# Optimization experiments

Hardware: AMD Instinct MI355X
Metric: run time of the kernel (lower is better)

The kernel has to match this reference:

```python
import jax, jax.numpy as jnp
import numpy as np

B, S, DM = 2, 2048, 2048
H, KV, HD = 16, 4, 128
THETA = 10000.0
EPS = 1e-6


def _rmsnorm(x, scale):
    # flax nnx.RMSNorm with dtype=float32: x / sqrt(mean(x^2)+eps) * scale
    var = jnp.mean(jnp.square(x.astype(jnp.float32)), axis=-1, keepdims=True)
    return (x.astype(jnp.float32) * jax.lax.rsqrt(var + EPS)) * scale


def _apply_rope(x, positions, base):
    # x: [B, S, heads, HD]; positions: [1, S]
    half = HD // 2
    fraction = 2.0 * jnp.arange(half, dtype=jnp.float32) / HD
    timescale = base ** fraction                              # [HD/2]
    sinusoid = positions[..., None].astype(jnp.float32) / timescale  # [1, S, HD/2]
    sinusoid = sinusoid[..., None, :]                         # [1, S, 1, HD/2]
    sin, cos = jnp.sin(sinusoid), jnp.cos(sinusoid)
    x1, x2 = x[..., :half], x[..., half:]
    return jnp.concatenate([x1 * cos - x2 * sin, x2 * cos + x1 * sin], axis=-1).astype(x.dtype)


def setup_inputs() -> dict:
    key = jax.random.key(0)
    ks = jax.random.split(key, 7)
    w = lambda k, shape: jax.random.normal(k, shape, jnp.float32) * 0.02
    return {
        "x": jax.random.normal(ks[0], (B, S, DM), jnp.float32),
        "wq": w(ks[1], (DM, H, HD)),
        "wk": w(ks[2], (DM, KV, HD)),
        "wv": w(ks[3], (DM, KV, HD)),
        "wo": w(ks[4], (H, HD, DM)),
        "q_scale": jnp.ones((HD,), jnp.float32),
        "k_scale": jnp.ones((HD,), jnp.float32),
    }


def reference(x, wq, wk, wv, wo, q_scale, k_scale):
    # QKV projections (LinearGeneral hidden -> (heads, head_dim))
    q = jnp.einsum("bsd,dhk->bshk", x, wq)   # [B,S,H,HD]
    k = jnp.einsum("bsd,dhk->bshk", x, wk)   # [B,S,KV,HD]
    v = jnp.einsum("bsd,dhk->bshk", x, wv)   # [B,S,KV,HD]
    # qk RMSNorm + cast back to compute dtype
    q = _rmsnorm(q, q_scale).astype(x.dtype)
    k = _rmsnorm(k, k_scale).astype(x.dtype)
    # RoPE
    positions = jnp.arange(S)[None, :]
    q = _apply_rope(q, positions, THETA)
    k = _apply_rope(k, positions, THETA)
    # GQA attention: group query heads per kv head instead of materializing repeat_kv
    G = H // KV
    qg = q.reshape(B, S, KV, G, HD) * (HD ** -0.5)
    scores = jnp.einsum("bqkgd,bskd->bkgqs", qg, k)           # [B,KV,G,S,S]
    causal = jnp.tril(jnp.ones((S, S), jnp.bool_))
    scores = jnp.where(causal, scores, jnp.finfo(scores.dtype).min)
    probs = jax.nn.softmax(scores, axis=-1)
    att = jnp.einsum("bkgqs,bskd->bqkgd", probs, v).reshape(B, S, H, HD)
    # output projection contracting (heads, head_dim)
    return jnp.einsum("bshd,hdo->bso", att, wo)
```

## Files before the change

### kernel.cpp

```cpp
#include <hip/hip_runtime.h>
#include <hip/hip_bf16.h>
#include <math.h>

typedef unsigned short u16;
typedef short short8 __attribute__((ext_vector_type(8)));
typedef float floatx4 __attribute__((ext_vector_type(4)));

#define B_   2
#define S_   2048
#define DM_  2048
#define H_   16
#define KVH_ 4
#define HD_  128

__device__ __forceinline__ float bf2f(u16 v) {
  union { unsigned int u; float f; } x; x.u = ((unsigned int)v) << 16; return x.f;
}
__device__ __forceinline__ u16 f2bf(float f) {
  union { float f; unsigned int u; } x; x.f = f;
  unsigned int u = x.u;
  u += 0x7FFFu + ((u >> 16) & 1u);
  return (u16)(u >> 16);
}

#define GLDS16(gp, lp) __builtin_amdgcn_global_load_lds( \
    (const __attribute__((address_space(1))) unsigned int*)(const void*)(gp), \
    (__attribute__((address_space(3))) unsigned int*)(void*)(lp), 16, 0, 0)

__global__ __launch_bounds__(256) void k_prep(
    const float* __restrict__ x, const float* __restrict__ wq,
    const float* __restrict__ wk, const float* __restrict__ wv,
    const float* __restrict__ wo,
    u16* __restrict__ x_bf, u16* __restrict__ wqkv_t, u16* __restrict__ wo_t,
    float2* __restrict__ rope_tab)
{
  int bx = blockIdx.x;
  if (bx >= 18432) {
    int idx = (bx - 18432) * 256 + threadIdx.x;
    int pos = idx >> 6;
    float fi = (float)(idx & 63);
    float ts = powf(10000.0f, fi * (1.0f / 64.0f));
    float ang = (float)pos / ts;
    rope_tab[idx] = make_float2(cosf(ang), sinf(ang));
    return;
  }
  if (bx < 8192) {
    int i = bx * 256 + threadIdx.x;
    const float4 v = ((const float4*)x)[i];
    u16 o[4] = { f2bf(v.x), f2bf(v.y), f2bf(v.z), f2bf(v.w) };
    *(unsigned long long*)(x_bf + (size_t)i * 4) = *(unsigned long long*)o;
    return;
  }
  bx -= 8192;
  const float* src; u16* dst; int C, cb;
  if (bx < 4096)      { src = wq; dst = wqkv_t; C = 2048; cb = 64; }
  else if (bx < 5120) { bx -= 4096; src = wk; dst = wqkv_t + (size_t)2048 * 2048; C = 512; cb = 16; }
  else if (bx < 6144) { bx -= 5120; src = wv; dst = wqkv_t + (size_t)2560 * 2048; C = 512; cb = 16; }
  else                { bx -= 6144; src = wo; dst = wo_t; C = 2048; cb = 64; }
  const int R = 2048;
  int c0 = (bx % cb) * 32, r0 = (bx / cb) * 32;
  __shared__ float tile[32][33];
  int tx = threadIdx.x & 31, ty = threadIdx.x >> 5;
#pragma unroll
  for (int j = 0; j < 4; j++)
    tile[ty * 4 + j][tx] = src[(size_t)(r0 + ty * 4 + j) * C + c0 + tx];
  __syncthreads();
#pragma unroll
  for (int j = 0; j < 4; j++)
    dst[(size_t)(c0 + ty * 4 + j) * R + r0 + tx] = f2bf(tile[tx][ty * 4 + j]);
}

__global__ __launch_bounds__(256, 3) void k_gemm_bt(
    const u16* __restrict__ A, const u16* __restrict__ Bt,
    void* __restrict__ Cout, int M, int N, int K, int c_bf16)
{
  __shared__ u16 As[128 * 64];
  __shared__ u16 Bs[128 * 64];
  int tid = threadIdx.x;
  int lane = tid & 63;
  int quad = lane >> 4, l16 = lane & 15;
  int wid = tid >> 6;
  int m0 = blockIdx.y * 128, n0 = blockIdx.x * 128;
  int wm = (wid >> 1) * 64, wn = (wid & 1) * 64;

  floatx4 acc[4][4] = {};

  int srow = tid >> 3;
  int gjc0 = (tid & 7) ^ (srow & 7);
  const u16* Ap = A + (size_t)(m0 + srow) * K + gjc0 * 8;
  const u16* Bp = Bt + (size_t)(n0 + srow) * K + gjc0 * 8;
  u16* AsW = As + tid * 8;
  u16* BsW = Bs + tid * 8;

  for (int kt = 0; kt < K; kt += 64) {
    __syncthreads();
#pragma unroll
    for (int j = 0; j < 4; j++) {
      GLDS16(Ap + (size_t)(j * 32) * K, AsW + j * 2048);
      GLDS16(Bp + (size_t)(j * 32) * K, BsW + j * 2048);
    }
    Ap += 64; Bp += 64;
    __syncthreads();

#pragma unroll
    for (int ks = 0; ks < 2; ks++) {
      short8 af[4], bfv[4];
#pragma unroll
      for (int mi = 0; mi < 4; mi++) {
        int row = wm + mi * 16 + l16;
        af[mi] = *(const short8*)&As[row * 64 + (((ks * 4 + quad) ^ (row & 7)) * 8)];
      }
#pragma unroll
      for (int ni = 0; ni < 4; ni++) {
        int row = wn + ni * 16 + l16;
        bfv[ni] = *(const short8*)&Bs[row * 64 + (((ks * 4 + quad) ^ (row & 7)) * 8)];
      }
#pragma unroll
      for (int mi = 0; mi < 4; mi++)
#pragma unroll
        for (int ni = 0; ni < 4; ni++)
          acc[mi][ni] = __builtin_amdgcn_mfma_f32_16x16x32_bf16(
              af[mi], bfv[ni], acc[mi][ni], 0, 0, 0);
    }
  }

#pragma unroll
  for (int mi = 0; mi < 4; mi++)
#pragma unroll
    for (int ni = 0; ni < 4; ni++)
#pragma unroll
      for (int r = 0; r < 4; r++) {
        int row = m0 + wm + mi * 16 + quad * 4 + r;
        int col = n0 + wn + ni * 16 + l16;
        float v = acc[mi][ni][r];
        if (c_bf16) ((u16*)Cout)[(size_t)row * N + col] = f2bf(v);
        else        ((float*)Cout)[(size_t)row * N + col] = v;
      }
}

__global__ __launch_bounds__(256, 3) void k_gemm_qkv(
    const u16* __restrict__ A, const u16* __restrict__ Bt,
    const float* __restrict__ qs, const float* __restrict__ ks,
    const float2* __restrict__ tab,
    u16* __restrict__ qr, u16* __restrict__ kr, u16* __restrict__ vt)
{
  const int K = 2048;
  __shared__ u16 smem[16384] __attribute__((aligned(16)));
  u16* As = smem;
  u16* Bs = smem + 8192;
  float* exch = (float*)smem;

  int tid = threadIdx.x;
  int lane = tid & 63;
  int quad = lane >> 4, l16 = lane & 15;
  int wid = tid >> 6;
  int m0 = blockIdx.y * 128, n0 = blockIdx.x * 128;
  int wm = (wid >> 1) * 64, wn = (wid & 1) * 64;

  floatx4 acc[4][4] = {};

  int srow = tid >> 3;
  int gjc0 = (tid & 7) ^ (srow & 7);
  const u16* Ap = A + (size_t)(m0 + srow) * K + gjc0 * 8;
  const u16* Bp = Bt + (size_t)(n0 + srow) * K + gjc0 * 8;
  u16* AsW = As + tid * 8;
  u16* BsW = Bs + tid * 8;

  for (int kt = 0; kt < K; kt += 64) {
    __syncthreads();
#pragma unroll
    for (int j = 0; j < 4; j++) {
      GLDS16(Ap + (size_t)(j * 32) * K, AsW + j * 2048);
      GLDS16(Bp + (size_t)(j * 32) * K, BsW + j * 2048);
    }
    Ap += 64; Bp += 64;
    __syncthreads();

#pragma unroll
    for (int ks = 0; ks < 2; ks++) {
      short8 af[4], bfv[4];
#pragma unroll
      for (int mi = 0; mi < 4; mi++) {
        int row = wm + mi * 16 + l16;
        af[mi] = *(const short8*)&As[row * 64 + (((ks * 4 + quad) ^ (row & 7)) * 8)];
      }
#pragma unroll
      for (int ni = 0; ni < 4; ni++) {
        int row = wn + ni * 16 + l16;
        bfv[ni] = *(const short8*)&Bs[row * 64 + (((ks * 4 + quad) ^ (row & 7)) * 8)];
      }
#pragma unroll
      for (int mi = 0; mi < 4; mi++)
#pragma unroll
        for (int ni = 0; ni < 4; ni++)
          acc[mi][ni] = __builtin_amdgcn_mfma_f32_16x16x32_bf16(
              af[mi], bfv[ni], acc[mi][ni], 0, 0, 0);
    }
  }

  int nt = blockIdx.x;
  if (nt >= 20) {
    int kv = nt - 20;
    int b  = m0 >> 11;
    int s0 = m0 & (S_ - 1);
    __syncthreads();
#pragma unroll
    for (int mi = 0; mi < 4; mi++)
#pragma unroll
      for (int ni = 0; ni < 4; ni++)
#pragma unroll
        for (int r = 0; r < 4; r++) {
          int sl  = wm + mi * 16 + quad * 4 + r;
          int col = wn + ni * 16 + l16;
          smem[col * 128 + (((sl >> 3) ^ (col & 7)) * 8) + (sl & 7)] =
              f2bf(acc[mi][ni][r]);
        }
    __syncthreads();
    size_t vbase = ((size_t)(b * KVH_ + kv) * HD_) * S_ + s0;
#pragma unroll
    for (int i = 0; i < 8; i++) {
      int flat = i * 256 + tid;
      int hd = flat >> 4, sc = flat & 15;
      short8 vv = *(const short8*)&smem[hd * 128 + ((sc ^ (hd & 7)) * 8)];
      *(short8*)(vt + vbase + (size_t)hd * S_ + sc * 8) = vv;
    }
    return;
  }

  bool isq = nt < 16;
  const float* scp = isq ? qs : ks;
  float sc_own[4], sc_par[4];
#pragma unroll
  for (int ni = 0; ni < 4; ni++) {
    sc_own[ni] = scp[wn + ni * 16 + l16];
    sc_par[ni] = scp[(wn ^ 64) + ni * 16 + l16];
  }
  float ssign = (wn == 0) ? -1.0f : 1.0f;

#pragma unroll
  for (int mi = 0; mi < 4; mi++) {
    __syncthreads();
#pragma unroll
    for (int ni = 0; ni < 4; ni++)
#pragma unroll
      for (int r = 0; r < 4; r++)
        exch[(ni * 4 + r) * 256 + wid * 64 + lane] = acc[mi][ni][r];
    __syncthreads();
    float part[4][4];
#pragma unroll
    for (int ni = 0; ni < 4; ni++)
#pragma unroll
      for (int r = 0; r < 4; r++)
        part[ni][r] = exch[(ni * 4 + r) * 256 + (wid ^ 1) * 64 + lane];

#pragma unroll
    for (int r = 0; r < 4; r++) {
      float ss = 0.f;
#pragma unroll
      for (int ni = 0; ni < 4; ni++)
        ss += acc[mi][ni][r] * acc[mi][ni][r] + part[ni][r] * part[ni][r];
#pragma unroll
      for (int d = 1; d < 16; d <<= 1) ss += __shfl_xor(ss, d);
      float rs = rsqrtf(ss * (1.0f / 128.0f) + 1e-6f);
      int row = m0 + wm + mi * 16 + quad * 4 + r;
      int pos = row & (S_ - 1);
#pragma unroll
      for (int ni = 0; ni < 4; ni++) {
        float2 cs = tab[pos * 64 + ni * 16 + l16];
        float yo = acc[mi][ni][r] * rs * sc_own[ni];
        float yp = part[ni][r] * rs * sc_par[ni];
        float o = fmaf(ssign * yp, cs.y, yo * cs.x);
        if (isq) o *= 0.088388347648318447f;
        int d = wn + ni * 16 + l16;
        if (isq) qr[((size_t)row * H_ + nt) * HD_ + d] = f2bf(o);
        else     kr[((size_t)row * KVH_ + (nt - 16)) * HD_ + d] = f2bf(o);
      }
    }
  }
}

__global__ __launch_bounds__(256, 2) void k_flash(
    const u16* __restrict__ qr, const u16* __restrict__ kr,
    const u16* __restrict__ vt, u16* __restrict__ att)
{
  __shared__ u16 smem[40960] __attribute__((aligned(16)));
  u16* Ps = smem + 32768;
  float* lpbuf = (float*)(smem + 32768);

  int tid = threadIdx.x, lane = tid & 63, wid = tid >> 6;
  int quad = lane >> 4, l16 = lane & 15;
  int rhalf = wid & 1;
  int shalf = wid >> 1;
  int bx = blockIdx.x;
  int it = 31 - (bx >> 5);
  int hb = bx & 31;
  int h = hb & 15, b = hb >> 4;
  int kvh = h >> 2;
  int q0 = it * 64;
  int NT = it + 1;

  short8 qf[2][4];
#pragma unroll
  for (int m = 0; m < 2; m++) {
    const u16* qb = qr + ((size_t)(b * S_ + q0 + rhalf * 32 + m * 16 + l16) * H_ + h) * HD_;
#pragma unroll
    for (int kk = 0; kk < 4; kk++)
      qf[m][kk] = *(const short8*)(qb + kk * 32 + quad * 8);
  }

  int gjk = (tid & 15) ^ ((tid >> 4) & 15);
  int gjv = (tid & 7) ^ ((tid >> 3) & 7);
  const u16* kp = kr + ((size_t)(b * S_ + (tid >> 4)) * KVH_ + kvh) * HD_ + gjk * 8;
  const u16* vp = vt + ((size_t)(b * KVH_ + kvh) * HD_ + (tid >> 3)) * S_ + gjv * 8;

#pragma unroll
  for (int j = 0; j < 4; j++) {
    GLDS16(kp + (size_t)(j * 16) * KVH_ * HD_, smem + (size_t)(j * 256 + tid) * 8);
    GLDS16(vp + (size_t)(j * 32) * S_,         smem + 16384 + (size_t)(j * 256 + tid) * 8);
  }
  kp += (size_t)64 * KVH_ * HD_;
  vp += 64;
  __syncthreads();

  floatx4 accO[2][8] = {};
  float lp[2][4] = {};
  u16* PsW = Ps + wid * 2048;

  const float LOG2E = 1.4426950408889634f;
  const float MBIAS = -12.5f * 1.4426950408889634f;
  int qmax = q0 + rhalf * 32 + 31;

  for (int kt = 0; kt < NT; kt++) {
    if (kt + 1 < NT) {
      u16* KD = smem + (size_t)((kt + 1) & 1) * 8192;
      u16* VD = smem + 16384 + (size_t)((kt + 1) & 1) * 8192;
#pragma unroll
      for (int j = 0; j < 4; j++) {
        GLDS16(kp + (size_t)(j * 16) * KVH_ * HD_, KD + (size_t)(j * 256 + tid) * 8);
        GLDS16(vp + (size_t)(j * 32) * S_,         VD + (size_t)(j * 256 + tid) * 8);
      }
      kp += (size_t)64 * KVH_ * HD_;
      vp += 64;
    }

    int k0 = kt * 64;
    int s0w = k0 + shalf * 32;
    if (s0w <= qmax) {
      const u16* KsC = smem + (size_t)(kt & 1) * 8192;
      const u16* VtC = smem + 16384 + (size_t)(kt & 1) * 8192;

      floatx4 sacc[2][2] = {};
      __builtin_amdgcn_s_setprio(1);
#pragma unroll
      for (int kk = 0; kk < 4; kk++) {
        short8 kf[2];
#pragma unroll
        for (int nt = 0; nt < 2; nt++) {
          int row = shalf * 32 + nt * 16 + l16;
          kf[nt] = *(const short8*)&KsC[row * 128 + (((kk * 4 + quad) ^ (row & 15)) * 8)];
        }
#pragma unroll
        for (int nt = 0; nt < 2; nt++) {
          sacc[0][nt] = __builtin_amdgcn_mfma_f32_16x16x32_bf16(qf[0][kk], kf[nt], sacc[0][nt], 0, 0, 0);
          sacc[1][nt] = __builtin_amdgcn_mfma_f32_16x16x32_bf16(qf[1][kk], kf[nt], sacc[1][nt], 0, 0, 0);
        }
      }
      __builtin_amdgcn_s_setprio(0);

      bool diag = (s0w + 31 > q0 + rhalf * 32);
#pragma unroll
      for (int m = 0; m < 2; m++)
#pragma unroll
        for (int r = 0; r < 4; r++) {
          int prow = m * 16 + quad * 4 + r;
          int qrow = q0 + rhalf * 32 + prow;
          float rsum = 0.f;
#pragma unroll
          for (int nt = 0; nt < 2; nt++) {
            float p = __builtin_amdgcn_exp2f(fmaf(sacc[m][nt][r], LOG2E, MBIAS));
            if (diag && (s0w + nt * 16 + l16) > qrow) p = 0.f;
            rsum += p;
            int chunk = nt * 2 + (l16 >> 3);
            PsW[prow * 64 + ((chunk ^ (prow & 7)) * 8) + (l16 & 7)] = f2bf(p);
          }
          lp[m][r] += rsum;
        }

      __builtin_amdgcn_s_setprio(1);
      short8 pf[2];
#pragma unroll
      for (int m = 0; m < 2; m++) {
        int prow = m * 16 + l16;
        pf[m] = *(const short8*)&PsW[prow * 64 + ((quad ^ (prow & 7)) * 8)];
      }
#pragma unroll
      for (int ht = 0; ht < 8; ht++) {
        int row = ht * 16 + l16;
        short8 vf = *(const short8*)&VtC[row * 64 + (((shalf * 4 + quad) ^ (row & 7)) * 8)];
        accO[0][ht] = __builtin_amdgcn_mfma_f32_16x16x32_bf16(pf[0], vf, accO[0][ht], 0, 0, 0);
        accO[1][ht] = __builtin_amdgcn_mfma_f32_16x16x32_bf16(pf[1], vf, accO[1][ht], 0, 0, 0);
      }
      __builtin_amdgcn_s_setprio(0);
    }
    __syncthreads();
  }

#pragma unroll
  for (int m = 0; m < 2; m++)
#pragma unroll
    for (int r = 0; r < 4; r++) {
#pragma unroll
      for (int d = 1; d < 16; d <<= 1) lp[m][r] += __shfl_xor(lp[m][r], d);
    }

  floatx4* xch = (floatx4*)(void*)smem;
  if (wid >= 2) {
    floatx4* dst = xch + ((wid & 1) * 1024 + lane * 16);
#pragma unroll
    for (int m = 0; m < 2; m++)
#pragma unroll
      for (int ht = 0; ht < 8; ht++)
        dst[(m * 8 + ht + lane) & 15] = accO[m][ht];
    if (l16 == 0) {
#pragma unroll
      for (int m = 0; m < 2; m++)
#pragma unroll
        for (int r = 0; r < 4; r++)
          lpbuf[(wid & 1) * 32 + m * 16 + quad * 4 + r] = lp[m][r];
    }
  }
  __syncthreads();
  if (wid < 2) {
    floatx4* src = xch + (wid * 1024 + lane * 16);
    float inv[2][4];
#pragma unroll
    for (int m = 0; m < 2; m++)
#pragma unroll
      for (int ht = 0; ht < 8; ht++)
        accO[m][ht] += src[(m * 8 + ht + lane) & 15];
#pragma unroll
    for (int m = 0; m < 2; m++)
#pragma unroll
      for (int r = 0; r < 4; r++)
        inv[m][r] = 1.0f / (lp[m][r] + lpbuf[wid * 32 + m * 16 + quad * 4 + r]);
#pragma unroll
    for (int m = 0; m < 2; m++)
#pragma unroll
      for (int ht = 0; ht < 8; ht++)
#pragma unroll
        for (int r = 0; r < 4; r++) {
          int row = q0 + wid * 32 + m * 16 + quad * 4 + r;
          att[((size_t)(b * S_ + row) * H_ + h) * HD_ + ht * 16 + l16] =
              f2bf(accO[m][ht][r] * inv[m][r]);
        }
  }
}

extern "C" void kernel_launch(void* const* d_in, const int* in_sizes, int n_in,
                              void* d_out, int out_size, void* d_ws, size_t ws_size,
                              hipStream_t stream)
{
  const float* x  = (const float*)d_in[0];
  const float* wq = (const float*)d_in[1];
  const float* wk = (const float*)d_in[2];
  const float* wv = (const float*)d_in[3];
  const float* wo = (const float*)d_in[4];
  const float* qs = (const float*)d_in[5];
  const float* ks = (const float*)d_in[6];

  char* ws = (char*)d_ws;
  size_t off = 0;
  u16* x_bf   = (u16*)(ws + off); off += (size_t)4096 * 2048 * 2;
  u16* wqkv_t = (u16*)(ws + off); off += (size_t)3072 * 2048 * 2;
  u16* wo_t   = (u16*)(ws + off); off += (size_t)2048 * 2048 * 2;
  u16* q_rope = (u16*)(ws + off); off += (size_t)4096 * 16 * 128 * 2;
  u16* k_rope = (u16*)(ws + off); off += (size_t)4096 * 4 * 128 * 2;
  u16* vt     = (u16*)(ws + off); off += (size_t)8 * 128 * 2048 * 2;
  u16* att    = (u16*)(ws + off); off += (size_t)4096 * 2048 * 2;
  float2* rope_tab = (float2*)(ws + off); off += (size_t)2048 * 64 * 8;

  k_prep<<<dim3(18944), 256, 0, stream>>>(x, wq, wk, wv, wo, x_bf, wqkv_t, wo_t, rope_tab);

  k_gemm_qkv<<<dim3(24, 32), 256, 0, stream>>>(x_bf, wqkv_t, qs, ks, rope_tab,
                                               q_rope, k_rope, vt);

  k_flash<<<dim3(1024), 256, 0, stream>>>(q_rope, k_rope, vt, att);

  k_gemm_bt<<<dim3(16, 32), 256, 0, stream>>>(att, wo_t, d_out, 4096, 2048, 2048, 0);

  (void)in_sizes; (void)n_in; (void)out_size; (void)ws_size;
}
```

Before: 274.0 us.

## Keep softmax probabilities in registers by computing transposed S tile

Swaps MFMA operand order so each lane holds scores for one query row across consecutive keys, and permutes the K tile row loading so the register layout matches the PV MFMA A-operand. Probabilities are packed to bf16 with v_cvt_pk_bf16_f32 and fed directly to the PV MFMA, removing the per-wave LDS round trip for P and shrinking shared memory. Row sums become per-lane and need fewer shuffles, with a shuffle to redistribute them at the end. The risk is a subtle layout mismatch in the K-row permutation.

```diff
diff --git a/kernel.cpp b/kernel.cpp
--- a/kernel.cpp
+++ b/kernel.cpp
@@ -283,9 +283,8 @@
     const u16* __restrict__ qr, const u16* __restrict__ kr,
     const u16* __restrict__ vt, u16* __restrict__ att)
 {
-  __shared__ u16 smem[40960] __attribute__((aligned(16)));
-  u16* Ps = smem + 32768;
-  float* lpbuf = (float*)(smem + 32768);
+  __shared__ u16 smem[32768] __attribute__((aligned(16)));
+  float* lpbuf = (float*)(smem + 16384);
 
   int tid = threadIdx.x, lane = tid & 63, wid = tid >> 6;
   int quad = lane >> 4, l16 = lane & 15;
@@ -308,14 +307,17 @@
       qf[m][kk] = *(const short8*)(qb + kk * 32 + quad * 8);
   }
 
-  int gjk = (tid & 15) ^ ((tid >> 4) & 15);
+  int R0 = tid >> 4;
+  int base_act = (R0 >> 2) * 8 + (R0 & 3);
+  int gjk = (tid & 15) ^ (R0 & 15);
   int gjv = (tid & 7) ^ ((tid >> 3) & 7);
-  const u16* kp = kr + ((size_t)(b * S_ + (tid >> 4)) * KVH_ + kvh) * HD_ + gjk * 8;
+  const u16* kp = kr + ((size_t)(b * S_ + base_act) * KVH_ + kvh) * HD_ + gjk * 8;
   const u16* vp = vt + ((size_t)(b * KVH_ + kvh) * HD_ + (tid >> 3)) * S_ + gjv * 8;
+  const int joffK[4] = {0, 4, 32, 36};
 
 #pragma unroll
   for (int j = 0; j < 4; j++) {
-    GLDS16(kp + (size_t)(j * 16) * KVH_ * HD_, smem + (size_t)(j * 256 + tid) * 8);
+    GLDS16(kp + (size_t)joffK[j] * KVH_ * HD_, smem + (size_t)(j * 256 + tid) * 8);
     GLDS16(vp + (size_t)(j * 32) * S_,         smem + 16384 + (size_t)(j * 256 + tid) * 8);
   }
   kp += (size_t)64 * KVH_ * HD_;
@@ -323,12 +325,12 @@
   __syncthreads();
 
   floatx4 accO[2][8] = {};
-  float lp[2][4] = {};
-  u16* PsW = Ps + wid * 2048;
+  float lp[2] = { 0.f, 0.f };
 
   const float LOG2E = 1.4426950408889634f;
   const float MBIAS = -12.5f * 1.4426950408889634f;
   int qmax = q0 + rhalf * 32 + 31;
+  int qrow0 = q0 + rhalf * 32 + l16;
 
   for (int kt = 0; kt < NT; kt++) {
     if (kt + 1 < NT) {
@@ -336,7 +338,7 @@
       u16* VD = smem + 16384 + (size_t)((kt + 1) & 1) * 8192;
 #pragma unroll
       for (int j = 0; j < 4; j++) {
-        GLDS16(kp + (size_t)(j * 16) * KVH_ * HD_, KD + (size_t)(j * 256 + tid) * 8);
+        GLDS16(kp + (size_t)joffK[j] * KVH_ * HD_, KD + (size_t)(j * 256 + tid) * 8);
         GLDS16(vp + (size_t)(j * 32) * S_,         VD + (size_t)(j * 256 + tid) * 8);
       }
       kp += (size_t)64 * KVH_ * HD_;
@@ -361,38 +363,39 @@
         }
 #pragma unroll
         for (int nt = 0; nt < 2; nt++) {
-          sacc[0][nt] = __builtin_amdgcn_mfma_f32_16x16x32_bf16(qf[0][kk], kf[nt], sacc[0][nt], 0, 0, 0);
-          sacc[1][nt] = __builtin_amdgcn_mfma_f32_16x16x32_bf16(qf[1][kk], kf[nt], sacc[1][nt], 0, 0, 0);
+          sacc[0][nt] = __builtin_amdgcn_mfma_f32_16x16x32_bf16(kf[nt], qf[0][kk], sacc[0][nt], 0, 0, 0);
+          sacc[1][nt] = __builtin_amdgcn_mfma_f32_16x16x32_bf16(kf[nt], qf[1][kk], sacc[1][nt], 0, 0, 0);
         }
       }
       __builtin_amdgcn_s_setprio(0);
 
       bool diag = (s0w + 31 > q0 + rhalf * 32);
-#pragma unroll
-      for (int m = 0; m < 2; m++)
-#pragma unroll
-        for (int r = 0; r < 4; r++) {
-          int prow = m * 16 + quad * 4 + r;
-          int qrow = q0 + rhalf * 32 + prow;
-          float rsum = 0.f;
-#pragma unroll
-          for (int nt = 0; nt < 2; nt++) {
-            float p = __builtin_amdgcn_exp2f(fmaf(sacc[m][nt][r], LOG2E, MBIAS));
-            if (diag && (s0w + nt * 16 + l16) > qrow) p = 0.f;
+      int kb = s0w + quad * 8;
+      short8 pf[2];
+#pragma unroll
+      for (int m = 0; m < 2; m++) {
+        int qrow = qrow0 + m * 16;
+        float ps[8];
+        float rsum = 0.f;
+#pragma unroll
+        for (int nti = 0; nti < 2; nti++)
+#pragma unroll
+          for (int r = 0; r < 4; r++) {
+            float p = __builtin_amdgcn_exp2f(fmaf(sacc[m][nti][r], LOG2E, MBIAS));
+            if (diag && (kb + nti * 4 + r) > qrow) p = 0.f;
+            ps[nti * 4 + r] = p;
             rsum += p;
-            int chunk = nt * 2 + (l16 >> 3);
-            PsW[prow * 64 + ((chunk ^ (prow & 7)) * 8) + (l16 & 7)] = f2bf(p);
           }
-          lp[m][r] += rsum;
-        }
+        lp[m] += rsum;
+        union { unsigned int w[4]; short8 s; } pk_;
+#pragma unroll
+        for (int c = 0; c < 4; c++)
+          asm("v_cvt_pk_bf16_f32 %0, %1, %2"
+              : "=v"(pk_.w[c]) : "v"(ps[2 * c]), "v"(ps[2 * c + 1]));
+        pf[m] = pk_.s;
+      }
 
       __builtin_amdgcn_s_setprio(1);
-      short8 pf[2];
-#pragma unroll
-      for (int m = 0; m < 2; m++) {
-        int prow = m * 16 + l16;
-        pf[m] = *(const short8*)&PsW[prow * 64 + ((quad ^ (prow & 7)) * 8)];
-      }
 #pragma unroll
       for (int ht = 0; ht < 8; ht++) {
         int row = ht * 16 + l16;
@@ -406,12 +409,10 @@
   }
 
 #pragma unroll
-  for (int m = 0; m < 2; m++)
-#pragma unroll
-    for (int r = 0; r < 4; r++) {
-#pragma unroll
-      for (int d = 1; d < 16; d <<= 1) lp[m][r] += __shfl_xor(lp[m][r], d);
-    }
+  for (int m = 0; m < 2; m++) {
+    lp[m] += __shfl_xor(lp[m], 16);
+    lp[m] += __shfl_xor(lp[m], 32);
+  }
 
   floatx4* xch = (floatx4*)(void*)smem;
   if (wid >= 2) {
@@ -421,12 +422,10 @@
 #pragma unroll
       for (int ht = 0; ht < 8; ht++)
         dst[(m * 8 + ht + lane) & 15] = accO[m][ht];
-    if (l16 == 0) {
+    if (lane < 16) {
 #pragma unroll
       for (int m = 0; m < 2; m++)
-#pragma unroll
-        for (int r = 0; r < 4; r++)
-          lpbuf[(wid & 1) * 32 + m * 16 + quad * 4 + r] = lp[m][r];
+        lpbuf[(wid & 1) * 32 + m * 16 + lane] = lp[m];
     }
   }
   __syncthreads();
@@ -441,8 +440,10 @@
 #pragma unroll
     for (int m = 0; m < 2; m++)
 #pragma unroll
-      for (int r = 0; r < 4; r++)
-        inv[m][r] = 1.0f / (lp[m][r] + lpbuf[wid * 32 + m * 16 + quad * 4 + r]);
+      for (int r = 0; r < 4; r++) {
+        float own = __shfl(lp[m], quad * 4 + r);
+        inv[m][r] = 1.0f / (own + lpbuf[wid * 32 + m * 16 + quad * 4 + r]);
+      }
 #pragma unroll
     for (int m = 0; m < 2; m++)
 #pragma unroll
```

Measured after the change: 265.0 us. 1.03x faster.
